# Kernel tuning notes

Measured on AMD Instinct MI355X. Metric: run time of the kernel, lower is better.

## Reference

```python
import jax, jax.numpy as jnp
import numpy as np
from jax import lax

INPUT_SIZE = 512
STRIDES = (8, 16, 32)
NUM_CLASSES = 2
KA = 3  # anchors per scale
EPS = 1e-8
ANCHORS = np.array([[[10, 13], [16, 30], [33, 23]],
                    [[30, 61], [62, 45], [59, 119]],
                    [[116, 90], [156, 198], [373, 326]]], dtype=np.float32)

def _grid(stride):
    f = INPUT_SIZE // stride
    gy, gx = np.meshgrid(np.arange(f), np.arange(f), indexing='ij')
    return jnp.asarray(np.stack([gx, gy], -1).reshape(-1, 2).astype(np.float32))  # [HW,2] (x,y)

GRIDS = [_grid(s) for s in STRIDES]


def conv_ltc(x, conv_w, bn_gamma, bn_beta, cm, vleak, tau_m, e_revin):
    """Discrete LTC recurrence over time (tau_input=True, usetaum=True, stream_opt=True).
    x: [B,T,C,H,W] -> [B,T,Cout,H,W]"""
    B, T, C, H, W = x.shape
    Cout = conv_w.shape[0]

    def step(v_pre, xt):
        z = lax.conv_general_dilated(xt, conv_w, (1, 1), ((1, 1), (1, 1)),
                                     dimension_numbers=('NCHW', 'OIHW', 'NCHW'))
        wih = z * bn_gamma + bn_beta  # BatchNorm in eval form (per-channel affine)
        num = tau_m * v_pre / (vleak + cm * jax.nn.sigmoid(wih)) + wih * e_revin
        v = jax.nn.sigmoid(num / (1.0 + EPS))
        return v, v

    v0 = jnp.zeros((B, Cout, H, W), x.dtype)
    _, ys = lax.scan(step, v0, jnp.moveaxis(x, 1, 0))  # [T,B,Cout,H,W]
    return jnp.moveaxis(ys, 0, 1)


def head(y, w, b):
    # 1x1 conv detection head
    return jnp.einsum('bchw,oc->bohw', y, w) + b[None, :, None, None]


def decode_scale(pred, i):
    """pred: [B, KA*(1+C+4), h, w] -> obj [B,hw*KA,1], cls [B,hw*KA,C], box [B,hw*KA,4]."""
    B, _, h, w = pred.shape
    s = STRIDES[i]
    p = jnp.transpose(pred, (0, 2, 3, 1))  # [B,h,w,21]
    obj = p[..., :KA].reshape(B, -1, 1)
    cls = p[..., KA:KA * (1 + NUM_CLASSES)].reshape(B, -1, NUM_CLASSES)
    reg = p[..., KA * (1 + NUM_CLASSES):].reshape(B, h * w, KA, 4)
    anchors = jnp.asarray(ANCHORS[i])  # [KA,2]
    xy = (jax.nn.sigmoid(reg[..., :2]) + GRIDS[i][None, :, None, :]) * s
    wh = jnp.exp(reg[..., 2:]) * anchors[None, None, :, :]
    xywh = jnp.concatenate([xy, wh], -1).reshape(B, -1, 4)
    box = jnp.concatenate([xywh[..., :2] - xywh[..., 2:] * 0.5,
                           xywh[..., :2] + xywh[..., 2:] * 0.5], -1) / INPUT_SIZE
    return obj, cls, box


def setup_inputs() -> dict:
    key = jax.random.key(0)
    ks = jax.random.split(key, 12)
    B = 8
    x = jax.random.uniform(ks[0], (B, 5, 5, 512, 512), jnp.float32)
    y1 = jax.random.normal(ks[1], (B, 768, 16, 16), jnp.float32)
    y2 = jax.random.normal(ks[2], (B, 384, 32, 32), jnp.float32)
    y3 = jax.random.normal(ks[3], (B, 192, 64, 64), jnp.float32)
    conv_w = jax.random.normal(ks[4], (5, 5, 3, 3), jnp.float32) * 0.15  # xavier-ish
    bn_gamma = jnp.ones((5, 1, 1), jnp.float32)
    bn_beta = jnp.zeros((5, 1, 1), jnp.float32)
    cm = 1.0 + 0.1 * jax.random.normal(ks[5], (5, 1, 1), jnp.float32)
    vleak = 1.0 + 0.1 * jax.random.normal(ks[6], (5, 1, 1), jnp.float32)
    tau_m = 0.8 - 0.3 * jax.random.uniform(ks[7], (5, 1, 1), jnp.float32)
    e_revin = 1.0 + 0.1 * jax.random.normal(ks[8], (5, 1, 1), jnp.float32)
    OC = KA * (1 + NUM_CLASSES + 4)  # 21
    w1 = jax.random.normal(ks[9], (OC, 768), jnp.float32) * 0.02
    w2 = jax.random.normal(ks[10], (OC, 384), jnp.float32) * 0.02
    w3 = jax.random.normal(ks[11], (OC, 192), jnp.float32) * 0.02
    b1 = jnp.zeros((OC,), jnp.float32)
    b2 = jnp.zeros((OC,), jnp.float32)
    b3 = jnp.zeros((OC,), jnp.float32)
    return dict(x=x, y1=y1, y2=y2, y3=y3, conv_w=conv_w, bn_gamma=bn_gamma,
                bn_beta=bn_beta, cm=cm, vleak=vleak, tau_m=tau_m, e_revin=e_revin,
                w1=w1, b1=b1, w2=w2, b2=b2, w3=w3, b3=b3)


def reference(x, y1, y2, y3, conv_w, bn_gamma, bn_beta, cm, vleak, tau_m, e_revin,
              w1, b1, w2, b2, w3, b3):
    enc = conv_ltc(x, conv_w, bn_gamma, bn_beta, cm, vleak, tau_m, e_revin)
    # preds ordered [pred_s (y3, stride 8), pred_m (y2, 16), pred_l (y1, 32)]
    preds = [head(y3, w3, b3), head(y2, w2, b2), head(y1, w1, b1)]
    objs, clss, boxes = [], [], []
    for i, p in enumerate(preds):
        o, c, bx = decode_scale(p, i)
        objs.append(o); clss.append(c); boxes.append(bx)
    det = jnp.concatenate([jnp.concatenate(objs, 1),
                           jnp.concatenate(clss, 1),
                           jnp.concatenate(boxes, 1)], -1)  # [B, 16128, 7]
    return enc, det
```

## Files before the change

### kernel.cpp

```cpp
#include <hip/hip_runtime.h>
#include <math.h>

#define HH 512
#define WW 512
#define HWp (HH * WW)
#define TT 5
#define CC 5

#define CTW 64
#define CTH 16
#define NROW (CTH + 2)
#define GCOL 18
#define LCP (GCOL * 4)
#define LDSF (CC * NROW * LCP)
#define NG (CC * NROW * GCOL)
#define NBUF 3
#define SPARE_BYTES (NBUF * LDSF * 4)

typedef __attribute__((address_space(3))) char       lds_char_t;
typedef __attribute__((address_space(1)))  const char glb_char_t;

__device__ __forceinline__ float fast_sigmoid(float x) {
    return __builtin_amdgcn_rcpf(1.0f + __expf(-x));
}

extern "C" __global__ __launch_bounds__(512, 4)
void conv_ltc_kernel(const float* __restrict__ x, const float* __restrict__ cw,
                     const float* __restrict__ gamma, const float* __restrict__ beta,
                     const float* __restrict__ cm, const float* __restrict__ vleak,
                     const float* __restrict__ tau, const float* __restrict__ erev,
                     float* __restrict__ out)
{
    __shared__ float xs[NBUF * LDSF + 256];

    const int tid = threadIdx.x;
    const int bx = blockIdx.x;
    const int by = blockIdx.y;
    const int b  = blockIdx.z;

    const int grow0 = by * CTH;
    const int gcol0 = bx * CTW;
    const size_t xb = (size_t)b * (TT * CC * HWp);

    int  goff[4];
    bool pred[4];
    uint32_t gbase[4];
    #pragma unroll
    for (int k = 0; k < 4; ++k) {
        const int g = tid + k * 512;
        const int wavebase = (tid & ~63) + k * 512;
        if (wavebase >= NG) {
            pred[k] = true;
            goff[k] = 0;
            gbase[k] = (uint32_t)SPARE_BYTES;
        } else {
            const bool valid = g < NG;
            const int gg  = valid ? g : 0;
            const int ch  = gg / (NROW * GCOL);
            const int rem = gg - ch * (NROW * GCOL);
            const int row = rem / GCOL;
            const int c4  = rem - row * GCOL;
            const int gr = grow0 + row - 1;
            const int gc = gcol0 - 4 + c4 * 4;
            const bool inb = valid && ((unsigned)gr < (unsigned)HH) && ((unsigned)gc < (unsigned)WW);
            pred[k] = inb;
            goff[k] = ch * HWp + gr * WW + gc;
            gbase[k] = (uint32_t)(wavebase * 16);
            if (valid && !inb) {
                float4 z = make_float4(0.f, 0.f, 0.f, 0.f);
                *(float4*)&xs[g * 4]            = z;
                *(float4*)&xs[LDSF + g * 4]     = z;
                *(float4*)&xs[2 * LDSF + g * 4] = z;
            }
        }
    }

    lds_char_t* lds0 = (lds_char_t*)xs;

    auto issue_stage = [&](int t, int buf) {
        const float* xt = x + xb + (size_t)t * (CC * HWp);
        const uint32_t bufoff = (uint32_t)buf * (LDSF * 4);
        #pragma unroll
        for (int k = 0; k < 4; ++k) {
            if (pred[k]) {
                __builtin_amdgcn_global_load_lds(
                    (const __attribute__((address_space(1))) void*)(glb_char_t*)(const char*)(xt + goff[k]),
                    (__attribute__((address_space(3))) void*)(lds0 + bufoff + gbase[k]),
                    16, 0, 0);
            }
        }
    };

    float g_[CC], be[CC], cmv[CC], vl[CC], tm[CC], er[CC];
    #pragma unroll
    for (int o = 0; o < CC; ++o) {
        g_[o] = gamma[o]; be[o] = beta[o]; cmv[o] = cm[o];
        vl[o] = vleak[o]; tm[o] = tau[o]; er[o] = erev[o];
    }

    const int tx = tid & 63;
    const int r0 = (tid >> 6) * 2;

    issue_stage(0, 0);
    issue_stage(1, 1);
    asm volatile("s_waitcnt vmcnt(4)" ::: "memory");
    asm volatile("s_waitcnt lgkmcnt(0)" ::: "memory");
    __builtin_amdgcn_s_barrier();
    __builtin_amdgcn_sched_barrier(0);

    float vpre[2][CC];
    #pragma unroll
    for (int r = 0; r < 2; ++r)
        #pragma unroll
        for (int o = 0; o < CC; ++o) vpre[r][o] = 0.0f;

    #pragma unroll
    for (int t = 0; t < TT; ++t) {
        if (t + 2 < TT) issue_stage(t + 2, (t + 2) % NBUF);

        const float* cur = xs + (t % NBUF) * LDSF;

        float acc[2][CC];
        #pragma unroll
        for (int r = 0; r < 2; ++r)
            #pragma unroll
            for (int o = 0; o < CC; ++o) acc[r][o] = 0.0f;

        #pragma unroll
        for (int ic = 0; ic < CC; ++ic) {
            float rv[4][3];
            #pragma unroll
            for (int dr = 0; dr < 4; ++dr) {
                const float* lp = &cur[(ic * NROW + (r0 + dr)) * LCP + tx + 3];
                rv[dr][0] = lp[0]; rv[dr][1] = lp[1]; rv[dr][2] = lp[2];
            }
            #pragma unroll
            for (int oc = 0; oc < CC; ++oc) {
                const float* wp = cw + (oc * CC + ic) * 9;
                float wv[9];
                #pragma unroll
                for (int k = 0; k < 9; ++k) wv[k] = wp[k];
                float a0 = acc[0][oc], a1 = acc[1][oc];
                #pragma unroll
                for (int dr = 0; dr < 3; ++dr)
                    #pragma unroll
                    for (int dc = 0; dc < 3; ++dc) {
                        a0 = fmaf(wv[dr * 3 + dc], rv[dr][dc],     a0);
                        a1 = fmaf(wv[dr * 3 + dc], rv[dr + 1][dc], a1);
                    }
                acc[0][oc] = a0; acc[1][oc] = a1;
            }
        }

        #pragma unroll
        for (int r = 0; r < 2; ++r) {
            const int grow = grow0 + r0 + r;
            const size_t ob = (size_t)grow * WW + gcol0 + tx;
            #pragma unroll
            for (int o = 0; o < CC; ++o) {
                float wih = fmaf(acc[r][o], g_[o], be[o]);
                float sg  = fast_sigmoid(wih);
                float den = fmaf(cmv[o], sg, vl[o]);
                float num = fmaf(tm[o] * vpre[r][o], __builtin_amdgcn_rcpf(den), wih * er[o]);
                float v   = fast_sigmoid(num);
                vpre[r][o] = v;
                out[((size_t)((b * TT + t) * CC + o)) * HWp + ob] = v;
            }
        }

        if (t <= 2) {
            asm volatile("s_waitcnt vmcnt(14)" ::: "memory");
            __builtin_amdgcn_s_barrier();
            __builtin_amdgcn_sched_barrier(0);
        } else if (t == 3) {
            asm volatile("s_waitcnt vmcnt(10)" ::: "memory");
            __builtin_amdgcn_s_barrier();
            __builtin_amdgcn_sched_barrier(0);
        }
    }
}

#define SMEM_F 18432

extern "C" __global__ __launch_bounds__(512)
void head_fused_kernel(const float* __restrict__ y3, const float* __restrict__ w3, const float* __restrict__ b3,
                       const float* __restrict__ y2, const float* __restrict__ w2, const float* __restrict__ b2,
                       const float* __restrict__ y1, const float* __restrict__ w1, const float* __restrict__ b1,
                       float* __restrict__ det)
{
    __shared__ float smem[SMEM_F];

    const int bid = blockIdx.x;
    const float *y, *w, *bias;
    int Cin, f, lgf, lgchunks, row_off;
    float s;
    float aw0, aw1, aw2, ah0, ah1, ah2;
    int sb;

    if (bid < 512) {
        sb = bid;       y = y3; w = w3; bias = b3; Cin = 192; f = 64; lgf = 6; lgchunks = 6; s = 8.0f;  row_off = 0;
        aw0 = 10.f;  ah0 = 13.f;  aw1 = 16.f;  ah1 = 30.f;  aw2 = 33.f;  ah2 = 23.f;
    } else if (bid < 640) {
        sb = bid - 512; y = y2; w = w2; bias = b2; Cin = 384; f = 32; lgf = 5; lgchunks = 4; s = 16.0f; row_off = 12288;
        aw0 = 30.f;  ah0 = 61.f;  aw1 = 62.f;  ah1 = 45.f;  aw2 = 59.f;  ah2 = 119.f;
    } else {
        sb = bid - 640; y = y1; w = w1; bias = b1; Cin = 768; f = 16; lgf = 4; lgchunks = 2; s = 32.0f; row_off = 15360;
        aw0 = 116.f; ah0 = 90.f;  aw1 = 156.f; ah1 = 198.f; aw2 = 373.f; ah2 = 326.f;
    }

    const int n     = f * f;
    const int b     = sb >> lgchunks;
    const int chunk = sb & ((1 << lgchunks) - 1);

    const int tid  = threadIdx.x;
    const int lane = tid & 63;
    const int grp  = tid >> 6;

    const int wtot = Cin * 21;
    for (int i = tid; i < wtot; i += 512) {
        int o = i / Cin;
        int c = i - o * Cin;
        smem[c * 24 + o] = w[i];
    }
    __syncthreads();

    const int G   = Cin >> 3;
    const int pix = (chunk << 6) + lane;

    float acc[21];
    #pragma unroll
    for (int o = 0; o < 21; ++o) acc[o] = 0.0f;

    const float* yp = y + ((size_t)b * Cin + (size_t)grp * G) * n + pix;
    const int wbase = grp * G * 24;

    #pragma unroll 4
    for (int c = 0; c < G; ++c) {
        float v = yp[(size_t)c * n];
        const float* wr = &smem[wbase + c * 24];
        float4 q0 = *(const float4*)(wr);
        float4 q1 = *(const float4*)(wr + 4);
        float4 q2 = *(const float4*)(wr + 8);
        float4 q3 = *(const float4*)(wr + 12);
        float4 q4 = *(const float4*)(wr + 16);
        float  s20 = wr[20];
        float wv[21] = {q0.x,q0.y,q0.z,q0.w, q1.x,q1.y,q1.z,q1.w,
                        q2.x,q2.y,q2.z,q2.w, q3.x,q3.y,q3.z,q3.w,
                        q4.x,q4.y,q4.z,q4.w, s20};
        #pragma unroll
        for (int o = 0; o < 21; ++o) acc[o] = fmaf(v, wv[o], acc[o]);
    }
    __syncthreads();

    #pragma unroll
    for (int o = 0; o < 21; ++o) smem[tid * 21 + o] = acc[o];
    __syncthreads();

    if (tid < 64) {
        float r[21];
        #pragma unroll
        for (int o = 0; o < 21; ++o) r[o] = bias[o];
        #pragma unroll
        for (int g2 = 0; g2 < 8; ++g2) {
            const float* rp = &smem[(g2 * 64 + lane) * 21];
            #pragma unroll
            for (int o = 0; o < 21; ++o) r[o] += rp[o];
        }

        const int hy = pix >> lgf;
        const int hx = pix & (f - 1);
        const float inv = 1.0f / 512.0f;
        const float AW[3] = {aw0, aw1, aw2};
        const float AH[3] = {ah0, ah1, ah2};

        #pragma unroll
        for (int a = 0; a < 3; ++a) {
            const int row = row_off + pix * 3 + a;
            float* dp = det + ((size_t)b * 16128 + row) * 7;
            dp[0] = r[a];
            dp[1] = r[3 + a * 2];
            dp[2] = r[4 + a * 2];
            float txv = r[9  + a * 4];
            float tyv = r[10 + a * 4];
            float twv = r[11 + a * 4];
            float thv = r[12 + a * 4];
            float cx = (fast_sigmoid(txv) + (float)hx) * s;
            float cy = (fast_sigmoid(tyv) + (float)hy) * s;
            float bw = __expf(twv) * AW[a];
            float bh = __expf(thv) * AH[a];
            dp[3] = (cx - bw * 0.5f) * inv;
            dp[4] = (cy - bh * 0.5f) * inv;
            dp[5] = (cx + bw * 0.5f) * inv;
            dp[6] = (cy + bh * 0.5f) * inv;
        }
    }
}

extern "C" void kernel_launch(void* const* d_in, const int* in_sizes, int n_in,
                              void* d_out, int out_size, void* d_ws, size_t ws_size,
                              hipStream_t stream)
{
    const float* x     = (const float*)d_in[0];
    const float* y1    = (const float*)d_in[1];
    const float* y2    = (const float*)d_in[2];
    const float* y3    = (const float*)d_in[3];
    const float* cw    = (const float*)d_in[4];
    const float* gamma = (const float*)d_in[5];
    const float* beta  = (const float*)d_in[6];
    const float* cm    = (const float*)d_in[7];
    const float* vleak = (const float*)d_in[8];
    const float* tau   = (const float*)d_in[9];
    const float* erev  = (const float*)d_in[10];
    const float* w1    = (const float*)d_in[11];
    const float* b1    = (const float*)d_in[12];
    const float* w2    = (const float*)d_in[13];
    const float* b2    = (const float*)d_in[14];
    const float* w3    = (const float*)d_in[15];
    const float* b3    = (const float*)d_in[16];

    float* out = (float*)d_out;
    float* det = out + (size_t)8 * TT * CC * HH * WW;

    dim3 cgrid(WW / CTW, HH / CTH, 8);
    conv_ltc_kernel<<<cgrid, 512, 0, stream>>>(x, cw, gamma, beta, cm, vleak, tau, erev, out);

    head_fused_kernel<<<dim3(672), 512, 0, stream>>>(y3, w3, b3, y2, w2, b2, y1, w1, b1, det);
}
```

Baseline: 169.4 us.

## Use packed v2f FMAs in the LTC conv with duplicated weight table

The conv weights are copied into a duplicated-pair global table by a small extra kernel so the 3x3 conv can use packed two-lane FMAs (v_pk_fma_f32). Each thread now computes two columns 32 apart in a single row, instead of two adjacent rows in one column. This is meant to halve the FMA instruction count in the conv inner loop. It costs one extra kernel launch, loses the vertical row reuse (each thread now does 3 LDS row loads per input channel instead of 4 shared between two rows), and reads weights from a global table rather than the input pointer.

Result: slower. 443.8 us (+162.0%).

```diff
diff --git a/kernel.cpp b/kernel.cpp
--- a/kernel.cpp
+++ b/kernel.cpp
@@ -17,15 +17,28 @@
 #define NBUF 3
 #define SPARE_BYTES (NBUF * LDSF * 4)
 
+typedef float v2f __attribute__((ext_vector_type(2)));
+
 typedef __attribute__((address_space(3))) char       lds_char_t;
 typedef __attribute__((address_space(1)))  const char glb_char_t;
 
+__device__ float WDUP[450];
+
 __device__ __forceinline__ float fast_sigmoid(float x) {
     return __builtin_amdgcn_rcpf(1.0f + __expf(-x));
 }
 
+extern "C" __global__ void repack_w_kernel(const float* __restrict__ cw) {
+    const int i = threadIdx.x;
+    if (i < 225) {
+        float w = cw[i];
+        WDUP[2 * i]     = w;
+        WDUP[2 * i + 1] = w;
+    }
+}
+
 extern "C" __global__ __launch_bounds__(512, 4)
-void conv_ltc_kernel(const float* __restrict__ x, const float* __restrict__ cw,
+void conv_ltc_kernel(const float* __restrict__ x,
                      const float* __restrict__ gamma, const float* __restrict__ beta,
                      const float* __restrict__ cm, const float* __restrict__ vleak,
                      const float* __restrict__ tau, const float* __restrict__ erev,
@@ -98,8 +111,8 @@
         vl[o] = vleak[o]; tm[o] = tau[o]; er[o] = erev[o];
     }
 
-    const int tx = tid & 63;
-    const int r0 = (tid >> 6) * 2;
+    const int cx = tid & 31;
+    const int ty = tid >> 5;
 
     issue_stage(0, 0);
     issue_stage(1, 1);
@@ -108,11 +121,11 @@
     __builtin_amdgcn_s_barrier();
     __builtin_amdgcn_sched_barrier(0);
 
-    float vpre[2][CC];
-    #pragma unroll
-    for (int r = 0; r < 2; ++r)
-        #pragma unroll
-        for (int o = 0; o < CC; ++o) vpre[r][o] = 0.0f;
+    float vpre0[CC], vpre1[CC];
+    #pragma unroll
+    for (int o = 0; o < CC; ++o) { vpre0[o] = 0.0f; vpre1[o] = 0.0f; }
+
+    const int rowbase = (grow0 + ty) * WW + gcol0;
 
     #pragma unroll
     for (int t = 0; t < TT; ++t) {
@@ -120,52 +133,49 @@
 
         const float* cur = xs + (t % NBUF) * LDSF;
 
-        float acc[2][CC];
-        #pragma unroll
-        for (int r = 0; r < 2; ++r)
+        v2f acc[CC];
+        #pragma unroll
+        for (int o = 0; o < CC; ++o) acc[o] = (v2f){0.0f, 0.0f};
+
+        #pragma unroll
+        for (int ic = 0; ic < CC; ++ic) {
             #pragma unroll
-            for (int o = 0; o < CC; ++o) acc[r][o] = 0.0f;
-
-        #pragma unroll
-        for (int ic = 0; ic < CC; ++ic) {
-            float rv[4][3];
-            #pragma unroll
-            for (int dr = 0; dr < 4; ++dr) {
-                const float* lp = &cur[(ic * NROW + (r0 + dr)) * LCP + tx + 3];
-                rv[dr][0] = lp[0]; rv[dr][1] = lp[1]; rv[dr][2] = lp[2];
+            for (int dr = 0; dr < 3; ++dr) {
+                const float* lp = &cur[(ic * NROW + ty + dr) * LCP + cx];
+                v2f xv0 = (v2f){lp[3], lp[35]};
+                v2f xv1 = (v2f){lp[4], lp[36]};
+                v2f xv2 = (v2f){lp[5], lp[37]};
+                #pragma unroll
+                for (int oc = 0; oc < CC; ++oc) {
+                    const v2f* wp = (const v2f*)&WDUP[2 * ((oc * CC + ic) * 9 + dr * 3)];
+                    v2f a = acc[oc];
+                    a = __builtin_elementwise_fma(wp[0], xv0, a);
+                    a = __builtin_elementwise_fma(wp[1], xv1, a);
+                    a = __builtin_elementwise_fma(wp[2], xv2, a);
+                    acc[oc] = a;
+                }
             }
-            #pragma unroll
-            for (int oc = 0; oc < CC; ++oc) {
-                const float* wp = cw + (oc * CC + ic) * 9;
-                float wv[9];
-                #pragma unroll
-                for (int k = 0; k < 9; ++k) wv[k] = wp[k];
-                float a0 = acc[0][oc], a1 = acc[1][oc];
-                #pragma unroll
-                for (int dr = 0; dr < 3; ++dr)
-                    #pragma unroll
-                    for (int dc = 0; dc < 3; ++dc) {
-                        a0 = fmaf(wv[dr * 3 + dc], rv[dr][dc],     a0);
-                        a1 = fmaf(wv[dr * 3 + dc], rv[dr + 1][dc], a1);
-                    }
-                acc[0][oc] = a0; acc[1][oc] = a1;
-            }
-        }
-
-        #pragma unroll
-        for (int r = 0; r < 2; ++r) {
-            const int grow = grow0 + r0 + r;
-            const size_t ob = (size_t)grow * WW + gcol0 + tx;
-            #pragma unroll
-            for (int o = 0; o < CC; ++o) {
-                float wih = fmaf(acc[r][o], g_[o], be[o]);
-                float sg  = fast_sigmoid(wih);
-                float den = fmaf(cmv[o], sg, vl[o]);
-                float num = fmaf(tm[o] * vpre[r][o], __builtin_amdgcn_rcpf(den), wih * er[o]);
-                float v   = fast_sigmoid(num);
-                vpre[r][o] = v;
-                out[((size_t)((b * TT + t) * CC + o)) * HWp + ob] = v;
-            }
+        }
+
+        #pragma unroll
+        for (int o = 0; o < CC; ++o) {
+            float* op = out + ((size_t)((b * TT + t) * CC + o)) * HWp + rowbase;
+
+            float wih0 = fmaf(acc[o].x, g_[o], be[o]);
+            float sg0  = fast_sigmoid(wih0);
+            float den0 = fmaf(cmv[o], sg0, vl[o]);
+            float num0 = fmaf(tm[o] * vpre0[o], __builtin_amdgcn_rcpf(den0), wih0 * er[o]);
+            float v0   = fast_sigmoid(num0);
+            vpre0[o] = v0;
+            op[cx] = v0;
+
+            float wih1 = fmaf(acc[o].y, g_[o], be[o]);
+            float sg1  = fast_sigmoid(wih1);
+            float den1 = fmaf(cmv[o], sg1, vl[o]);
+            float num1 = fmaf(tm[o] * vpre1[o], __builtin_amdgcn_rcpf(den1), wih1 * er[o]);
+            float v1   = fast_sigmoid(num1);
+            vpre1[o] = v1;
+            op[cx + 32] = v1;
         }
 
         if (t <= 2) {
@@ -321,8 +331,10 @@
     float* out = (float*)d_out;
     float* det = out + (size_t)8 * TT * CC * HH * WW;
 
+    repack_w_kernel<<<dim3(1), 256, 0, stream>>>(cw);
+
     dim3 cgrid(WW / CTW, HH / CTH, 8);
-    conv_ltc_kernel<<<cgrid, 512, 0, stream>>>(x, cw, gamma, beta, cm, vleak, tau, erev, out);
+    conv_ltc_kernel<<<cgrid, 512, 0, stream>>>(x, gamma, beta, cm, vleak, tau, erev, out);
 
     head_fused_kernel<<<dim3(672), 512, 0, stream>>>(y3, w3, b3, y2, w2, b2, y1, w1, b1, det);
 }
```
